# Performance work log

Measured on AMD Instinct MI355X. Metric: run time of the kernel, lower is better.

The kernel has to match this reference:

```python
import jax, jax.numpy as jnp
import numpy as np

B, S = 1, 1536
D_MODEL, NHEAD, HEAD_DIM = 1024, 16, 64
ROPE, NUM_SEQ = 32, 4
KVC, QC, D_FF = 256, 384, 4096
SPP = S // NUM_SEQ                      # seq per stock = 384
EPS_RMS = 1.1920929e-07                 # torch RMSNorm default eps = finfo(fp32).eps
ATTN_EPS = 1e-5
LAMBDA_INIT = 0.8 - 0.6 * float(np.exp(-0.3 * 0.0))  # depth 0 -> 0.2
SCALING = float(((HEAD_DIM + ROPE) // 2) ** -0.5)


def rmsnorm(x, w, eps=EPS_RMS):
    var = jnp.mean(jnp.square(x), axis=-1, keepdims=True)
    return x * jax.lax.rsqrt(var + eps) * w


def setup_inputs() -> dict:
    key = jax.random.key(0)
    ks = jax.random.split(key, 16)
    sd = 0.02
    inv_freq = 1.0 / (10000.0 ** (np.arange(0, ROPE // 4) / (ROPE // 4)))
    ang = np.arange(1, SPP)[:, None] * inv_freq[None, :]  # [SPP-1, ROPE//4]
    return {
        "x": jax.random.normal(ks[0], (B, S, D_MODEL), jnp.float32),
        "freqs_cos": jnp.asarray(np.cos(ang), jnp.float32),
        "freqs_sin": jnp.asarray(np.sin(ang), jnp.float32),
        "norm1_w": jnp.ones((D_MODEL,), jnp.float32),
        "norm2_w": jnp.ones((D_MODEL,), jnp.float32),
        "kv_down_w": jax.random.normal(ks[1], (KVC + ROPE, D_MODEL), jnp.float32) * sd,
        "q_down_w": jax.random.normal(ks[2], (QC, D_MODEL), jnp.float32) * sd,
        "kv_norm_w": jnp.ones((KVC,), jnp.float32),
        "q_norm_w": jnp.ones((QC,), jnp.float32),
        "kv_up_w": jax.random.normal(ks[3], (HEAD_DIM * NHEAD * 2, KVC), jnp.float32) * sd,
        "q_up_w": jax.random.normal(ks[4], ((HEAD_DIM + ROPE) * NHEAD, QC), jnp.float32) * sd,
        "lambda_q1": jax.random.normal(ks[5], (HEAD_DIM // 2,), jnp.float32) * 0.1,
        "lambda_k1": jax.random.normal(ks[6], (HEAD_DIM // 2,), jnp.float32) * 0.1,
        "lambda_q2": jax.random.normal(ks[7], (HEAD_DIM // 2,), jnp.float32) * 0.1,
        "lambda_k2": jax.random.normal(ks[8], (HEAD_DIM // 2,), jnp.float32) * 0.1,
        "attn_norm_w": jnp.ones((HEAD_DIM,), jnp.float32),
        "o_w": jax.random.normal(ks[9], (D_MODEL, NHEAD * HEAD_DIM), jnp.float32) * sd,
        "ff_in_w": jax.random.normal(ks[10], (D_FF * 2, D_MODEL), jnp.float32) * sd,
        "ff_out_w": jax.random.normal(ks[11], (D_MODEL, D_FF), jnp.float32) * sd,
    }


def reference(x, freqs_cos, freqs_sin, norm1_w, norm2_w, kv_down_w, q_down_w,
              kv_norm_w, q_norm_w, kv_up_w, q_up_w, lambda_q1, lambda_k1,
              lambda_q2, lambda_k2, attn_norm_w, o_w, ff_in_w, ff_out_w):
    b, s, _ = x.shape
    spp = s // NUM_SEQ
    H2, hd2 = 2 * NHEAD, HEAD_DIM // 2

    # block-tiled causal mask (1 = masked), matching mask.repeat(..., num_seq, num_seq)
    base = jnp.triu(jnp.ones((spp, spp), jnp.float32), 1)
    mask = jnp.tile(base, (NUM_SEQ, NUM_SEQ))  # [S, S]

    xin = rmsnorm(x, norm1_w)
    ckv = xin @ kv_down_w.T                                    # [B,S,KVC+ROPE]
    c_kv, k_rope = ckv[..., :KVC], ckv[..., KVC:]
    kv = (rmsnorm(c_kv, kv_norm_w) @ kv_up_w.T).reshape(b, s, NHEAD, 2 * HEAD_DIM)
    k, v = kv[..., :HEAD_DIM], kv[..., HEAD_DIM:]
    k = k.reshape(b, s, H2, hd2)
    qf = (rmsnorm(xin @ q_down_w.T, q_norm_w) @ q_up_w.T).reshape(b, s, NHEAD, HEAD_DIM + ROPE)
    q, q_rope = qf[..., :HEAD_DIM], qf[..., HEAD_DIM:]
    q = q.reshape(b, s, H2, hd2)
    k_rope = jnp.tile(k_rope[:, :, None, :], (1, 1, NHEAD, 1)).reshape(b, s, H2, ROPE // 2)
    q_rope = q_rope.reshape(b, s, H2, ROPE // 2)

    # rotary emb; position 0 of every ticker is left untouched (identity rotation)
    cos = jnp.concatenate([jnp.ones((1, ROPE // 4), freqs_cos.dtype), freqs_cos], 0)  # [spp, ROPE//4]
    sin = jnp.concatenate([jnp.zeros((1, ROPE // 4), freqs_sin.dtype), freqs_sin], 0)

    def rot(r):
        # S is laid out as (position, ticker) interleaved: s = p*NUM_SEQ + t
        r = r.reshape(b, spp, NUM_SEQ, H2, ROPE // 4, 2)
        c = cos[None, :, None, None, :]
        s_ = sin[None, :, None, None, :]
        r0, r1 = r[..., 0], r[..., 1]
        y = jnp.stack([r0 * c - r1 * s_, r0 * s_ + r1 * c], axis=-1)
        return y.reshape(b, s, H2, ROPE // 2)

    q = jnp.concatenate([q, rot(q_rope)], -1).transpose(0, 2, 1, 3)  # [B,2H,S,dk]
    k = jnp.concatenate([k, rot(k_rope)], -1).transpose(0, 2, 1, 3)
    v = v.transpose(0, 2, 1, 3)                                      # [B,H,S,hd]

    a = jnp.einsum('bhqd,bhkd->bhqk', q, k) * SCALING
    a = jnp.where(mask[None, None] == 1, -1e9, a)
    a = jax.nn.softmax(a, axis=-1)

    lam = jnp.exp(jnp.sum(lambda_k1 * lambda_q1)) - jnp.exp(jnp.sum(lambda_k2 * lambda_q2)) + LAMBDA_INIT
    a = a.reshape(b, NHEAD, 2, s, s)
    a1, a2 = a[:, :, 0], a[:, :, 1]
    g = jnp.mean(a1, axis=-2, keepdims=True)            # [B,H,1,S], broadcasts over queries
    a = a1 - lam * a2 + lam * g
    a = jnp.where(mask[None, None] == 1, 0.0, a)

    out = jnp.einsum('bhqk,bhkd->bhqd', a, v)           # [B,H,S,hd]
    out = rmsnorm(out.transpose(0, 2, 1, 3), attn_norm_w, eps=ATTN_EPS).transpose(0, 2, 1, 3)
    # faithful to source: raw reshape of [B,H,S,hd] -> [B,S,H*hd] (transposes cancel)
    out = out.reshape(b, s, NHEAD * HEAD_DIM)
    x = x + out @ o_w.T

    h = rmsnorm(x, norm2_w)
    uv = h @ ff_in_w.T
    u, vg = uv[..., :D_FF], uv[..., D_FF:]
    return x + (u * jax.nn.silu(vg)) @ ff_out_w.T
```

## Files before the change

### kernel.cpp

```cpp
#include <hip/hip_runtime.h>
#include <math.h>

#define S     1536
#define DM    1024
#define NH    16
#define H2N   32
#define HD    64
#define KVC   256
#define QC    384
#define DFF   4096
#define SPP   384
#define DQK   48
#define CKW   672
#define EPS_RMS  1.1920929e-07f
#define ATTN_EPS 1e-5f
#define SCALING  0.14433756729740643f

typedef float f32x4 __attribute__((ext_vector_type(4)));
typedef float f32x16 __attribute__((ext_vector_type(16)));
typedef short bf16x8 __attribute__((ext_vector_type(8)));

__device__ __forceinline__ short cvt_bf16(float f) {
  union { float f; unsigned u; } x; x.f = f;
  unsigned r = x.u + 0x7FFFu + ((x.u >> 16) & 1u);
  return (short)(r >> 16);
}
__device__ __forceinline__ unsigned pk2(float a, float b) {
  unsigned r;
  asm("v_cvt_pk_bf16_f32 %0, %1, %2" : "=v"(r) : "v"(a), "v"(b));
  return r;
}
__device__ __forceinline__ bf16x8 cvt8(float4 a, float4 b) {
  union { unsigned u[4]; bf16x8 v; } r;
  r.u[0] = pk2(a.x, a.y); r.u[1] = pk2(a.z, a.w);
  r.u[2] = pk2(b.x, b.y); r.u[3] = pk2(b.z, b.w);
  return r.v;
}
__device__ __forceinline__ int swz8(int flat, int nwg) {
  if (nwg & 7) return flat;
  return (flat & 7) * (nwg >> 3) + (flat >> 3);
}

__device__ __forceinline__ void rms_body(const float* xr, const float* w,
    short* yr, int cols, float eps) {
  const int tid = threadIdx.x;
  float ss = 0.f;
  for (int c = tid << 2; c < cols; c += 1024) {
    float4 v = *reinterpret_cast<const float4*>(xr + c);
    ss += v.x*v.x + v.y*v.y + v.z*v.z + v.w*v.w;
  }
#pragma unroll
  for (int mm = 1; mm < 64; mm <<= 1) ss += __shfl_xor(ss, mm, 64);
  __shared__ float red[4];
  if ((tid & 63) == 0) red[tid >> 6] = ss;
  __syncthreads();
  float tot = red[0] + red[1] + red[2] + red[3];
  float scale = rsqrtf(tot / (float)cols + eps);
  for (int c = tid << 2; c < cols; c += 1024) {
    float4 v = *reinterpret_cast<const float4*>(xr + c);
    float4 wv = *reinterpret_cast<const float4*>(w + c);
    uint2 p;
    p.x = pk2(v.x*scale*wv.x, v.y*scale*wv.y);
    p.y = pk2(v.z*scale*wv.z, v.w*scale*wv.w);
    *reinterpret_cast<uint2*>(yr + c) = p;
  }
}

__global__ __launch_bounds__(256) void rms1_cvt(const float* __restrict__ x,
    const float* __restrict__ n1w, short* __restrict__ xin_bf,
    const float* __restrict__ s0, int n0, const float* __restrict__ s1, int n1,
    const float* __restrict__ s2, int n2, const float* __restrict__ s3,
    short* __restrict__ dst) {
  const int bx = blockIdx.x;
  if (bx < S) {
    rms_body(x + (size_t)bx * DM, n1w, xin_bf + (size_t)bx * DM, DM, EPS_RMS);
  } else {
    long base = (long)(bx - S) * 2048 + (long)threadIdx.x * 8;
    const float* src; long off;
    if (base < n0) { src = s0; off = base; }
    else if (base < (long)n0 + n1) { src = s1; off = base - n0; }
    else if (base < (long)n0 + n1 + n2) { src = s2; off = base - n0 - n1; }
    else { src = s3; off = base - n0 - n1 - n2; }
    float4 a = *reinterpret_cast<const float4*>(src + off);
    float4 b = *reinterpret_cast<const float4*>(src + off + 4);
    *reinterpret_cast<bf16x8*>(dst + base) = cvt8(a, b);
  }
}

__global__ __launch_bounds__(256) void rmsnorm2_bf(const float* __restrict__ comb,
    const float* __restrict__ w0, const float* __restrict__ w1,
    short* __restrict__ o0, short* __restrict__ o1, float eps) {
  const int row = blockIdx.x;
  const int seg = blockIdx.y;
  const float* xr = comb + (size_t)row * CKW + (seg ? 288 : 0);
  rms_body(xr, seg ? w1 : w0,
           seg ? (o1 + (size_t)row * QC) : (o0 + (size_t)row * KVC),
           seg ? QC : KVC, eps);
}

__global__ __launch_bounds__(256) void rmsnorm_sum_bf(const float* __restrict__ p0,
    const float* __restrict__ p1, const float* __restrict__ xres,
    const float* __restrict__ w, float* __restrict__ outw, short* __restrict__ yb,
    float eps) {
  const int row = blockIdx.x;
  const int c = threadIdx.x << 2;
  const size_t base = (size_t)row * DM + c;
  float4 a = *reinterpret_cast<const float4*>(p0 + base);
  float4 b = *reinterpret_cast<const float4*>(p1 + base);
  float4 xv = *reinterpret_cast<const float4*>(xres + base);
  float4 v = make_float4(a.x+b.x+xv.x, a.y+b.y+xv.y, a.z+b.z+xv.z, a.w+b.w+xv.w);
  *reinterpret_cast<float4*>(outw + base) = v;
  float ss = v.x*v.x + v.y*v.y + v.z*v.z + v.w*v.w;
#pragma unroll
  for (int mm = 1; mm < 64; mm <<= 1) ss += __shfl_xor(ss, mm, 64);
  __shared__ float red[4];
  if ((threadIdx.x & 63) == 0) red[threadIdx.x >> 6] = ss;
  __syncthreads();
  float tot = red[0] + red[1] + red[2] + red[3];
  float scale = rsqrtf(tot * (1.0f / (float)DM) + eps);
  float4 wv = *reinterpret_cast<const float4*>(w + c);
  uint2 p;
  p.x = pk2(v.x*scale*wv.x, v.y*scale*wv.y);
  p.y = pk2(v.z*scale*wv.z, v.w*scale*wv.w);
  *reinterpret_cast<uint2*>(yb + base) = p;
}

__global__ __launch_bounds__(256) void fadd2(float* __restrict__ out,
    const float* __restrict__ p0, const float* __restrict__ p1) {
  size_t i = ((size_t)blockIdx.x * 256 + threadIdx.x) << 2;
  float4 o = *reinterpret_cast<float4*>(out + i);
  float4 a = *reinterpret_cast<const float4*>(p0 + i);
  float4 b = *reinterpret_cast<const float4*>(p1 + i);
  o.x += a.x + b.x; o.y += a.y + b.y; o.z += a.z + b.z; o.w += a.w + b.w;
  *reinterpret_cast<float4*>(out + i) = o;
}

template<int ADD>
__global__ __launch_bounds__(256) void mgemm_nt(const short* __restrict__ A,
    const short* __restrict__ B, const float* __restrict__ src, float* __restrict__ C,
    int M, int N, int K, int lda, int ldb, int ldc) {
  __shared__ short As[64][72];
  __shared__ short Bs[64][72];
  const int nwg = gridDim.x * gridDim.y;
  const int sfl = swz8(blockIdx.y * gridDim.x + blockIdx.x, nwg);
  const int bxs = sfl % gridDim.x, bys = sfl / gridDim.x;
  const int bm = bys * 64, bn = bxs * 64;
  const int tid = threadIdx.x;
  const int w = tid >> 6, lane = tid & 63;
  const int wr = (w >> 1) << 5, wc = (w & 1) << 5;
  const int srow = tid >> 2, sk = (tid & 3) << 4;
  const int lrow = lane & 15, lk8 = (lane >> 4) << 3;
  const int arow = bm + srow, brow = bn + srow;
  const bool bvalid = brow < N;
  f32x4 acc[2][2];
#pragma unroll
  for (int i = 0; i < 2; ++i)
#pragma unroll
    for (int j = 0; j < 2; ++j) acc[i][j] = (f32x4){0.f, 0.f, 0.f, 0.f};

  bf16x8 rah0, rah1, rbh0, rbh1;
  {
    const short* ap = A + (size_t)arow * lda + sk;
    rah0 = *reinterpret_cast<const bf16x8*>(ap);
    rah1 = *reinterpret_cast<const bf16x8*>(ap + 8);
  }
  rbh0 = (bf16x8){0,0,0,0,0,0,0,0}; rbh1 = rbh0;
  if (bvalid) {
    const short* bp = B + (size_t)brow * ldb + sk;
    rbh0 = *reinterpret_cast<const bf16x8*>(bp);
    rbh1 = *reinterpret_cast<const bf16x8*>(bp + 8);
  }

  for (int k0 = 0; k0 < K; k0 += 64) {
    bf16x8 va0 = rah0, va1 = rah1, vb0 = rbh0, vb1 = rbh1;
    __syncthreads();
    *reinterpret_cast<bf16x8*>(&As[srow][sk])     = va0;
    *reinterpret_cast<bf16x8*>(&As[srow][sk + 8]) = va1;
    *reinterpret_cast<bf16x8*>(&Bs[srow][sk])     = vb0;
    *reinterpret_cast<bf16x8*>(&Bs[srow][sk + 8]) = vb1;
    __syncthreads();
    const int kn = k0 + 64;
    if (kn < K) {
      const short* ap = A + (size_t)arow * lda + kn + sk;
      rah0 = *reinterpret_cast<const bf16x8*>(ap);
      rah1 = *reinterpret_cast<const bf16x8*>(ap + 8);
      if (bvalid) {
        const short* bp = B + (size_t)brow * ldb + kn + sk;
        rbh0 = *reinterpret_cast<const bf16x8*>(bp);
        rbh1 = *reinterpret_cast<const bf16x8*>(bp + 8);
      }
    }
#pragma unroll
    for (int kk = 0; kk < 2; ++kk) {
      bf16x8 af0 = *reinterpret_cast<bf16x8*>(&As[wr + lrow][(kk << 5) + lk8]);
      bf16x8 af1 = *reinterpret_cast<bf16x8*>(&As[wr + 16 + lrow][(kk << 5) + lk8]);
      bf16x8 bf0 = *reinterpret_cast<bf16x8*>(&Bs[wc + lrow][(kk << 5) + lk8]);
      bf16x8 bf1 = *reinterpret_cast<bf16x8*>(&Bs[wc + 16 + lrow][(kk << 5) + lk8]);
      acc[0][0] = __builtin_amdgcn_mfma_f32_16x16x32_bf16(af0, bf0, acc[0][0], 0, 0, 0);
      acc[0][1] = __builtin_amdgcn_mfma_f32_16x16x32_bf16(af0, bf1, acc[0][1], 0, 0, 0);
      acc[1][0] = __builtin_amdgcn_mfma_f32_16x16x32_bf16(af1, bf0, acc[1][0], 0, 0, 0);
      acc[1][1] = __builtin_amdgcn_mfma_f32_16x16x32_bf16(af1, bf1, acc[1][1], 0, 0, 0);
    }
  }
  const int crow0 = bm + wr + ((lane >> 4) << 2);
  const int ccol0 = bn + wc + lrow;
#pragma unroll
  for (int mi = 0; mi < 2; ++mi)
#pragma unroll
    for (int ni = 0; ni < 2; ++ni) {
      int colc = ccol0 + (ni << 4);
      if (colc < N) {
#pragma unroll
        for (int r = 0; r < 4; ++r) {
          int rowc = crow0 + (mi << 4) + r;
          float v = acc[mi][ni][r];
          if (ADD) v += src[(size_t)rowc * ldc + colc];
          C[(size_t)rowc * ldc + colc] = v;
        }
      }
    }
}

__global__ __launch_bounds__(256) void mgemm_dual(const short* __restrict__ A0,
    const short* __restrict__ B0, float* __restrict__ C0,
    const short* __restrict__ A1, const short* __restrict__ B1, float* __restrict__ C1) {
  __shared__ short As[64][72];
  __shared__ short Bs[64][72];
  const int flat = blockIdx.x;
  const short *A, *B; float* C;
  int K, lda, ldb, ldc, bm, bn;
  if (flat < 768) {
    const int sfl = swz8(flat, 768);
    bm = (sfl / 32) * 64; bn = (sfl % 32) * 64;
    A = A0; B = B0; C = C0; K = KVC; lda = KVC; ldb = KVC; ldc = 2048;
  } else {
    const int sfl = swz8(flat - 768, 576);
    bm = (sfl / 24) * 64; bn = (sfl % 24) * 64;
    A = A1; B = B1; C = C1; K = QC; lda = QC; ldb = QC; ldc = 1536;
  }
  const int tid = threadIdx.x;
  const int w = tid >> 6, lane = tid & 63;
  const int wr = (w >> 1) << 5, wc = (w & 1) << 5;
  const int srow = tid >> 2, sk = (tid & 3) << 4;
  const int lrow = lane & 15, lk8 = (lane >> 4) << 3;
  const int arow = bm + srow, brow = bn + srow;
  f32x4 acc[2][2];
#pragma unroll
  for (int i = 0; i < 2; ++i)
#pragma unroll
    for (int j = 0; j < 2; ++j) acc[i][j] = (f32x4){0.f, 0.f, 0.f, 0.f};

  bf16x8 rah0, rah1, rbh0, rbh1;
  {
    const short* ap = A + (size_t)arow * lda + sk;
    rah0 = *reinterpret_cast<const bf16x8*>(ap);
    rah1 = *reinterpret_cast<const bf16x8*>(ap + 8);
    const short* bp = B + (size_t)brow * ldb + sk;
    rbh0 = *reinterpret_cast<const bf16x8*>(bp);
    rbh1 = *reinterpret_cast<const bf16x8*>(bp + 8);
  }
  for (int k0 = 0; k0 < K; k0 += 64) {
    bf16x8 va0 = rah0, va1 = rah1, vb0 = rbh0, vb1 = rbh1;
    __syncthreads();
    *reinterpret_cast<bf16x8*>(&As[srow][sk])     = va0;
    *reinterpret_cast<bf16x8*>(&As[srow][sk + 8]) = va1;
    *reinterpret_cast<bf16x8*>(&Bs[srow][sk])     = vb0;
    *reinterpret_cast<bf16x8*>(&Bs[srow][sk + 8]) = vb1;
    __syncthreads();
    const int kn = k0 + 64;
    if (kn < K) {
      const short* ap = A + (size_t)arow * lda + kn + sk;
      rah0 = *reinterpret_cast<const bf16x8*>(ap);
      rah1 = *reinterpret_cast<const bf16x8*>(ap + 8);
      const short* bp = B + (size_t)brow * ldb + kn + sk;
      rbh0 = *reinterpret_cast<const bf16x8*>(bp);
      rbh1 = *reinterpret_cast<const bf16x8*>(bp + 8);
    }
#pragma unroll
    for (int kk = 0; kk < 2; ++kk) {
      bf16x8 af0 = *reinterpret_cast<bf16x8*>(&As[wr + lrow][(kk << 5) + lk8]);
      bf16x8 af1 = *reinterpret_cast<bf16x8*>(&As[wr + 16 + lrow][(kk << 5) + lk8]);
      bf16x8 bf0 = *reinterpret_cast<bf16x8*>(&Bs[wc + lrow][(kk << 5) + lk8]);
      bf16x8 bf1 = *reinterpret_cast<bf16x8*>(&Bs[wc + 16 + lrow][(kk << 5) + lk8]);
      acc[0][0] = __builtin_amdgcn_mfma_f32_16x16x32_bf16(af0, bf0, acc[0][0], 0, 0, 0);
      acc[0][1] = __builtin_amdgcn_mfma_f32_16x16x32_bf16(af0, bf1, acc[0][1], 0, 0, 0);
      acc[1][0] = __builtin_amdgcn_mfma_f32_16x16x32_bf16(af1, bf0, acc[1][0], 0, 0, 0);
      acc[1][1] = __builtin_amdgcn_mfma_f32_16x16x32_bf16(af1, bf1, acc[1][1], 0, 0, 0);
    }
  }
  const int crow0 = bm + wr + ((lane >> 4) << 2);
  const int ccol0 = bn + wc + lrow;
#pragma unroll
  for (int mi = 0; mi < 2; ++mi)
#pragma unroll
    for (int ni = 0; ni < 2; ++ni) {
      int colc = ccol0 + (ni << 4);
#pragma unroll
      for (int r = 0; r < 4; ++r) {
        int rowc = crow0 + (mi << 4) + r;
        C[(size_t)rowc * ldc + colc] = acc[mi][ni][r];
      }
    }
}

__device__ __forceinline__ void sk_body(const short* __restrict__ A,
    const short* __restrict__ B, float* __restrict__ C,
    int bm, int bn, int koff, int K2, int lda, int ldb, int ldc) {
  __shared__ short As[64][72];
  __shared__ short Bs[64][72];
  const int tid = threadIdx.x;
  const int w = tid >> 6, lane = tid & 63;
  const int wr = (w >> 1) << 5, wc = (w & 1) << 5;
  const int srow = tid >> 2, sk = (tid & 3) << 4;
  const int lrow = lane & 15, lk8 = (lane >> 4) << 3;
  const int arow = bm + srow, brow = bn + srow;
  f32x4 acc[2][2];
#pragma unroll
  for (int i = 0; i < 2; ++i)
#pragma unroll
    for (int j = 0; j < 2; ++j) acc[i][j] = (f32x4){0.f, 0.f, 0.f, 0.f};

  bf16x8 rah0, rah1, rbh0, rbh1;
  {
    const short* ap = A + (size_t)arow * lda + koff + sk;
    rah0 = *reinterpret_cast<const bf16x8*>(ap);
    rah1 = *reinterpret_cast<const bf16x8*>(ap + 8);
    const short* bp = B + (size_t)brow * ldb + koff + sk;
    rbh0 = *reinterpret_cast<const bf16x8*>(bp);
    rbh1 = *reinterpret_cast<const bf16x8*>(bp + 8);
  }
  const int kend = koff + K2;
  for (int k0 = koff; k0 < kend; k0 += 64) {
    bf16x8 va0 = rah0, va1 = rah1, vb0 = rbh0, vb1 = rbh1;
    __syncthreads();
    *reinterpret_cast<bf16x8*>(&As[srow][sk])     = va0;
    *reinterpret_cast<bf16x8*>(&As[srow][sk + 8]) = va1;
    *reinterpret_cast<bf16x8*>(&Bs[srow][sk])     = vb0;
    *reinterpret_cast<bf16x8*>(&Bs[srow][sk + 8]) = vb1;
    __syncthreads();
    const int kn = k0 + 64;
    if (kn < kend) {
      const short* ap = A + (size_t)arow * lda + kn + sk;
      rah0 = *reinterpret_cast<const bf16x8*>(ap);
      rah1 = *reinterpret_cast<const bf16x8*>(ap + 8);
      const short* bp = B + (size_t)brow * ldb + kn + sk;
      rbh0 = *reinterpret_cast<const bf16x8*>(bp);
      rbh1 = *reinterpret_cast<const bf16x8*>(bp + 8);
    }
#pragma unroll
    for (int kk = 0; kk < 2; ++kk) {
      bf16x8 af0 = *reinterpret_cast<bf16x8*>(&As[wr + lrow][(kk << 5) + lk8]);
      bf16x8 af1 = *reinterpret_cast<bf16x8*>(&As[wr + 16 + lrow][(kk << 5) + lk8]);
      bf16x8 bf0 = *reinterpret_cast<bf16x8*>(&Bs[wc + lrow][(kk << 5) + lk8]);
      bf16x8 bf1 = *reinterpret_cast<bf16x8*>(&Bs[wc + 16 + lrow][(kk << 5) + lk8]);
      acc[0][0] = __builtin_amdgcn_mfma_f32_16x16x32_bf16(af0, bf0, acc[0][0], 0, 0, 0);
      acc[0][1] = __builtin_amdgcn_mfma_f32_16x16x32_bf16(af0, bf1, acc[0][1], 0, 0, 0);
      acc[1][0] = __builtin_amdgcn_mfma_f32_16x16x32_bf16(af1, bf0, acc[1][0], 0, 0, 0);
      acc[1][1] = __builtin_amdgcn_mfma_f32_16x16x32_bf16(af1, bf1, acc[1][1], 0, 0, 0);
    }
  }
  const int crow0 = bm + wr + ((lane >> 4) << 2);
  const int ccol0 = bn + wc + lrow;
#pragma unroll
  for (int mi = 0; mi < 2; ++mi)
#pragma unroll
    for (int ni = 0; ni < 2; ++ni) {
      int colc = ccol0 + (ni << 4);
#pragma unroll
      for (int r = 0; r < 4; ++r) {
        int rowc = crow0 + (mi << 4) + r;
        C[(size_t)rowc * ldc + colc] = acc[mi][ni][r];
      }
    }
}

__global__ __launch_bounds__(256) void mgemm_sk(const short* __restrict__ A,
    const short* __restrict__ B, float* __restrict__ P0, float* __restrict__ P1,
    int M, int N, int K2, int lda, int ldb, int ldc) {
  const int nwg = gridDim.x * gridDim.y;
  const int sfl = swz8(blockIdx.y * gridDim.x + blockIdx.x, nwg);
  sk_body(A, B, blockIdx.z ? P1 : P0, (sfl / gridDim.x) * 64,
          (sfl % gridDim.x) * 64, blockIdx.z * K2, K2, lda, ldb, ldc);
}

__global__ __launch_bounds__(256) void oproj_cvt(const short* __restrict__ A,
    const short* __restrict__ B, float* __restrict__ P0, float* __restrict__ P1,
    const float* __restrict__ ffow, short* __restrict__ ffow_bf) {
  const int bx = blockIdx.x;
  if (bx < 768) {
    const int z = bx >= 384;
    const int sfl = swz8(bx - (z ? 384 : 0), 384);
    sk_body(A, B, z ? P1 : P0, (sfl / 16) * 64, (sfl % 16) * 64,
            z * 512, 512, DM, DM, DM);
  } else {
    long base = (long)(bx - 768) * 2048 + (long)threadIdx.x * 8;
    float4 a = *reinterpret_cast<const float4*>(ffow + base);
    float4 b = *reinterpret_cast<const float4*>(ffow + base + 4);
    *reinterpret_cast<bf16x8*>(ffow_bf + base) = cvt8(a, b);
  }
}

__global__ __launch_bounds__(256) void mgemm_glu(const short* __restrict__ A,
    const short* __restrict__ Bw, short* __restrict__ C,
    int M, int N, int K, int lda, int ldb, int ldc) {
  __shared__ short As[128][72];
  __shared__ short Bu[64][72];
  __shared__ short Bv[64][72];
  const int nwg = gridDim.x * gridDim.y;
  const int sfl = swz8(blockIdx.y * gridDim.x + blockIdx.x, nwg);
  const int bxs = sfl % gridDim.x, bys = sfl / gridDim.x;
  const int bm = bys * 128, bn = bxs * 64;
  const int tid = threadIdx.x;
  const int w = tid >> 6, lane = tid & 63;
  const int wr = (w >> 1) << 6, wc = (w & 1) << 5;
  const int arow = bm + (tid >> 1), ac = (tid & 1) << 5;
  const int brow = bn + (tid >> 2), bc = (tid & 3) << 4;
  const int lrow = lane & 15, lk8 = (lane >> 4) << 3;
  f32x4 au[4][2], av[4][2];
#pragma unroll
  for (int i = 0; i < 4; ++i)
#pragma unroll
    for (int j = 0; j < 2; ++j) {
      au[i][j] = (f32x4){0.f, 0.f, 0.f, 0.f};
      av[i][j] = (f32x4){0.f, 0.f, 0.f, 0.f};
    }
  bf16x8 ra[4], ru[2], rv[2];
  {
    const short* ap = A + (size_t)arow * lda + ac;
    const short* up = Bw + (size_t)brow * ldb + bc;
    const short* vp = Bw + (size_t)(N + brow) * ldb + bc;
#pragma unroll
    for (int e = 0; e < 4; ++e) ra[e] = *reinterpret_cast<const bf16x8*>(ap + (e << 3));
    ru[0] = *reinterpret_cast<const bf16x8*>(up);
    ru[1] = *reinterpret_cast<const bf16x8*>(up + 8);
    rv[0] = *reinterpret_cast<const bf16x8*>(vp);
    rv[1] = *reinterpret_cast<const bf16x8*>(vp + 8);
  }
  for (int k0 = 0; k0 < K; k0 += 64) {
    __syncthreads();
#pragma unroll
    for (int e = 0; e < 4; ++e)
      *reinterpret_cast<bf16x8*>(&As[tid >> 1][ac + (e << 3)]) = ra[e];
    *reinterpret_cast<bf16x8*>(&Bu[tid >> 2][bc])     = ru[0];
    *reinterpret_cast<bf16x8*>(&Bu[tid >> 2][bc + 8]) = ru[1];
    *reinterpret_cast<bf16x8*>(&Bv[tid >> 2][bc])     = rv[0];
    *reinterpret_cast<bf16x8*>(&Bv[tid >> 2][bc + 8]) = rv[1];
    __syncthreads();
    const int kn = k0 + 64;
    if (kn < K) {
      const short* ap = A + (size_t)arow * lda + kn + ac;
      const short* up = Bw + (size_t)brow * ldb + kn + bc;
      const short* vp = Bw + (size_t)(N + brow) * ldb + kn + bc;
#pragma unroll
      for (int e = 0; e < 4; ++e) ra[e] = *reinterpret_cast<const bf16x8*>(ap + (e << 3));
      ru[0] = *reinterpret_cast<const bf16x8*>(up);
      ru[1] = *reinterpret_cast<const bf16x8*>(up + 8);
      rv[0] = *reinterpret_cast<const bf16x8*>(vp);
      rv[1] = *reinterpret_cast<const bf16x8*>(vp + 8);
    }
#pragma unroll
    for (int kk = 0; kk < 2; ++kk) {
      bf16x8 af[4], uf[2], vf[2];
#pragma unroll
      for (int i = 0; i < 4; ++i)
        af[i] = *reinterpret_cast<bf16x8*>(&As[wr + (i << 4) + lrow][(kk << 5) + lk8]);
#pragma unroll
      for (int j = 0; j < 2; ++j) {
        uf[j] = *reinterpret_cast<bf16x8*>(&Bu[wc + (j << 4) + lrow][(kk << 5) + lk8]);
        vf[j] = *reinterpret_cast<bf16x8*>(&Bv[wc + (j << 4) + lrow][(kk << 5) + lk8]);
      }
      __builtin_amdgcn_s_setprio(1);
#pragma unroll
      for (int i = 0; i < 4; ++i)
#pragma unroll
        for (int j = 0; j < 2; ++j) {
          au[i][j] = __builtin_amdgcn_mfma_f32_16x16x32_bf16(af[i], uf[j], au[i][j], 0, 0, 0);
          av[i][j] = __builtin_amdgcn_mfma_f32_16x16x32_bf16(af[i], vf[j], av[i][j], 0, 0, 0);
        }
      __builtin_amdgcn_s_setprio(0);
    }
  }
  const int crow0 = bm + wr + ((lane >> 4) << 2);
  const int ccol0 = bn + wc + lrow;
#pragma unroll
  for (int mi = 0; mi < 4; ++mi)
#pragma unroll
    for (int ni = 0; ni < 2; ++ni) {
      int colc = ccol0 + (ni << 4);
#pragma unroll
      for (int r = 0; r < 4; ++r) {
        int rowc = crow0 + (mi << 4) + r;
        float uu = au[mi][ni][r], vg = av[mi][ni][r];
        float sig = 1.0f / (1.0f + __expf(-vg));
        C[(size_t)rowc * ldc + colc] = cvt_bf16(uu * vg * sig);
      }
    }
}

__global__ __launch_bounds__(256) void prep_attn(const float* __restrict__ qf,
    const float* __restrict__ kvb, const float* __restrict__ ckv,
    const float* __restrict__ fc, const float* __restrict__ fs,
    short* __restrict__ Qb, short* __restrict__ Kb, short* __restrict__ Vt) {
  __shared__ short Ts[128][74];
  const int bx = blockIdx.x;
  if (bx < 192) {
    const int t = (bx % 6) * 256 + threadIdx.x;
    const int h2 = bx / 6;
    const int hh = h2 >> 1, par = h2 & 1;
    const float* qrow = qf + (size_t)t*1536 + hh*96;
    const float* krow = kvb + (size_t)t*2048 + hh*128;
    unsigned qu[24], ku[24];
#pragma unroll
    for (int xq = 0; xq < 8; ++xq) {
      float4 qv = *reinterpret_cast<const float4*>(qrow + par*32 + (xq<<2));
      float4 kv = *reinterpret_cast<const float4*>(krow + par*32 + (xq<<2));
      qu[xq*2]   = pk2(qv.x, qv.y); qu[xq*2+1] = pk2(qv.z, qv.w);
      ku[xq*2]   = pk2(kv.x, kv.y); ku[xq*2+1] = pk2(kv.z, kv.w);
    }
    int p = t >> 2;
    const float* qr = qrow + 64 + par*16;
    const float* kr = ckv + (size_t)t*CKW + 256 + par*16;
#pragma unroll
    for (int mq = 0; mq < 8; ++mq) {
      float c = 1.f, sn = 0.f;
      if (p > 0) { c = fc[(p-1)*8 + mq]; sn = fs[(p-1)*8 + mq]; }
      float q0 = qr[2*mq], q1 = qr[2*mq+1];
      qu[16 + mq] = pk2(q0*c - q1*sn, q0*sn + q1*c);
      float k0 = kr[2*mq], k1 = kr[2*mq+1];
      ku[16 + mq] = pk2(k0*c - k1*sn, k0*sn + k1*c);
    }
    unsigned* qo = (unsigned*)(Qb + ((size_t)h2*S + t)*DQK);
    unsigned* ko = (unsigned*)(Kb + ((size_t)h2*S + t)*DQK);
#pragma unroll
    for (int e = 0; e < 6; ++e) {
      *reinterpret_cast<uint4*>(qo + (e<<2)) = make_uint4(qu[e*4], qu[e*4+1], qu[e*4+2], qu[e*4+3]);
      *reinterpret_cast<uint4*>(ko + (e<<2)) = make_uint4(ku[e*4], ku[e*4+1], ku[e*4+2], ku[e*4+3]);
    }
  } else {
    const int f2 = bx - 192;
    const int hh = f2 % 16;
    const int t0 = (f2 / 16) << 7;
    const int tl = threadIdx.x >> 3, dp = (threadIdx.x & 7) << 3;
#pragma unroll
    for (int pass = 0; pass < 4; ++pass) {
      int t = t0 + (pass << 5) + tl;
      const float* vp = kvb + (size_t)t*2048 + hh*128 + 64 + dp;
      float4 a = *reinterpret_cast<const float4*>(vp);
      float4 b = *reinterpret_cast<const float4*>(vp + 4);
      *reinterpret_cast<bf16x8*>(&Ts[(pass << 5) + tl][dp]) = cvt8(a, b);
    }
    __syncthreads();
    for (int idx = threadIdx.x; idx < 1024; idx += 256) {
      int d = idx >> 4, tseg = (idx & 15) << 3;
      bf16x8 v;
#pragma unroll
      for (int e = 0; e < 8; ++e) v[e] = Ts[tseg + e][d];
      *reinterpret_cast<bf16x8*>(Vt + ((size_t)hh*HD + d)*S + t0 + tseg) = v;
    }
  }
}

__global__ __launch_bounds__(256) void flash_mfma(const short* __restrict__ Qb,
    const short* __restrict__ Kb, const short* __restrict__ Vg,
    float* __restrict__ Ob, float* __restrict__ rowm, float* __restrict__ rowl,
    float* __restrict__ Ob1a, float* __restrict__ Ob1b,
    float* __restrict__ rm1, float* __restrict__ rl1) {
  const int h2 = blockIdx.y;
  const int hh = h2 >> 1;
  const int z  = blockIdx.z;
  const int tid = threadIdx.x;
  const int w = tid >> 6, lane = tid & 63;
  const int ql = lane & 31, h = lane >> 5;
  const int cq = blockIdx.x / 3, k = blockIdx.x % 3;
  const int qi = k + 3*w;
  const int qbase = cq*SPP + (qi << 5);
  const int ri0w = qi << 5;

  __shared__ __align__(16) float Ot[4][32][36];

  bf16x8 qf0, qf1, qf2;
  {
    const short* qp = Qb + ((size_t)h2*S + qbase + ql)*DQK + (h << 3);
    qf0 = *reinterpret_cast<const bf16x8*>(qp);
    qf1 = *reinterpret_cast<const bf16x8*>(qp + 16);
    qf2 = *reinterpret_cast<const bf16x8*>(qp + 32);
  }
  const short* Kbase = Kb + (size_t)h2*S*DQK + (h << 3);
  const short* V0 = Vg + ((size_t)hh*HD + ql)*S + (h << 3);
  const short* V1 = Vg + ((size_t)hh*HD + 32 + ql)*S + (h << 3);

  float m = -1e30f, l = 0.f;
  f32x16 o0, o1;
#pragma unroll
  for (int r = 0; r < 16; ++r) { o0[r] = 0.f; o1[r] = 0.f; }

  for (int c = (z << 1); c < (z << 1) + 2; ++c) {
    for (int jr = 0; jr <= ri0w; jr += 32) {
      const int j0 = c*SPP + jr;
      const bool diag = (jr == ri0w);
      const short* kp = Kbase + (size_t)(j0 + ql)*DQK;
      bf16x8 kf0 = *reinterpret_cast<const bf16x8*>(kp);
      bf16x8 kf1 = *reinterpret_cast<const bf16x8*>(kp + 16);
      bf16x8 kf2 = *reinterpret_cast<const bf16x8*>(kp + 32);
      bf16x8 v00 = *reinterpret_cast<const bf16x8*>(V0 + j0);
      bf16x8 v01 = *reinterpret_cast<const bf16x8*>(V0 + j0 + 16);
      bf16x8 v10 = *reinterpret_cast<const bf16x8*>(V1 + j0);
      bf16x8 v11 = *reinterpret_cast<const bf16x8*>(V1 + j0 + 16);

      f32x16 st;
#pragma unroll
      for (int r = 0; r < 16; ++r) st[r] = 0.f;
      __builtin_amdgcn_s_setprio(1);
      st = __builtin_amdgcn_mfma_f32_32x32x16_bf16(kf0, qf0, st, 0, 0, 0);
      st = __builtin_amdgcn_mfma_f32_32x32x16_bf16(kf1, qf1, st, 0, 0, 0);
      st = __builtin_amdgcn_mfma_f32_32x32x16_bf16(kf2, qf2, st, 0, 0, 0);
      __builtin_amdgcn_s_setprio(0);

      if (diag) {
#pragma unroll
        for (int r = 0; r < 16; ++r) {
          int kl = (r & 3) + ((r >> 2) << 3) + (h << 2);
          st[r] = (kl <= ql) ? st[r] * SCALING : -1e30f;
        }
      } else {
#pragma unroll
        for (int r = 0; r < 16; ++r) st[r] *= SCALING;
      }

      float tm = st[0];
#pragma unroll
      for (int r = 1; r < 16; ++r) tm = fmaxf(tm, st[r]);
      tm = fmaxf(tm, __shfl_xor(tm, 32));
      if (__any(tm > m + 8.0f)) {
        float mnew = fmaxf(m, tm);
        float sc = __expf(m - mnew);
        m = mnew;
        l *= sc;
#pragma unroll
        for (int r = 0; r < 16; ++r) { o0[r] *= sc; o1[r] *= sc; }
      }
      float ps = 0.f;
#pragma unroll
      for (int r = 0; r < 16; ++r) { float p = __expf(st[r] - m); st[r] = p; ps += p; }
      ps += __shfl_xor(ps, 32);
      l += ps;

      unsigned A0 = pk2(st[0],  st[1]),  B0 = pk2(st[2],  st[3]);
      unsigned C0 = pk2(st[4],  st[5]),  D0 = pk2(st[6],  st[7]);
      unsigned A1 = pk2(st[8],  st[9]),  B1 = pk2(st[10], st[11]);
      unsigned C1 = pk2(st[12], st[13]), D1 = pk2(st[14], st[15]);
      unsigned xA0 = (unsigned)__shfl_xor((int)A0, 32), xB0 = (unsigned)__shfl_xor((int)B0, 32);
      unsigned xC0 = (unsigned)__shfl_xor((int)C0, 32), xD0 = (unsigned)__shfl_xor((int)D0, 32);
      unsigned xA1 = (unsigned)__shfl_xor((int)A1, 32), xB1 = (unsigned)__shfl_xor((int)B1, 32);
      unsigned xC1 = (unsigned)__shfl_xor((int)C1, 32), xD1 = (unsigned)__shfl_xor((int)D1, 32);
      union { unsigned u[4]; bf16x8 v; } P0, P1;
      P0.u[0] = h ? xC0 : A0;  P0.u[1] = h ? xD0 : B0;
      P0.u[2] = h ? C0 : xA0;  P0.u[3] = h ? D0 : xB0;
      P1.u[0] = h ? xC1 : A1;  P1.u[1] = h ? xD1 : B1;
      P1.u[2] = h ? C1 : xA1;  P1.u[3] = h ? D1 : xB1;

      __builtin_amdgcn_s_setprio(1);
      o0 = __builtin_amdgcn_mfma_f32_32x32x16_bf16(v00, P0.v, o0, 0, 0, 0);
      o0 = __builtin_amdgcn_mfma_f32_32x32x16_bf16(v01, P1.v, o0, 0, 0, 0);
      o1 = __builtin_amdgcn_mfma_f32_32x32x16_bf16(v10, P0.v, o1, 0, 0, 0);
      o1 = __builtin_amdgcn_mfma_f32_32x32x16_bf16(v11, P1.v, o1, 0, 0, 0);
      __builtin_amdgcn_s_setprio(0);
    }
  }

  float* ot = &Ot[w][0][0];
  float* orow;
  if (z == 0) orow = Ob + ((size_t)h2*S + qbase)*HD;
  else orow = (h2 < 16) ? Ob1a + ((size_t)h2*S + qbase)*HD
                        : Ob1b + ((size_t)(h2 - 16)*S + qbase)*HD;
#pragma unroll
  for (int r = 0; r < 16; ++r) {
    int dl = (r & 3) + ((r >> 2) << 3) + (h << 2);
    ot[ql*36 + dl] = o0[r];
  }
#pragma unroll
  for (int it = 0; it < 4; ++it) {
    int idx = lane + (it << 6);
    int row = idx >> 3, c4 = (idx & 7) << 2;
    float4 v = *reinterpret_cast<float4*>(&ot[row*36 + c4]);
    *reinterpret_cast<float4*>(&orow[(size_t)row*HD + c4]) = v;
  }
#pragma unroll
  for (int r = 0; r < 16; ++r) {
    int dl = (r & 3) + ((r >> 2) << 3) + (h << 2);
    ot[ql*36 + dl] = o1[r];
  }
#pragma unroll
  for (int it = 0; it < 4; ++it) {
    int idx = lane + (it << 6);
    int row = idx >> 3, c4 = (idx & 7) << 2;
    float4 v = *reinterpret_cast<float4*>(&ot[row*36 + c4]);
    *reinterpret_cast<float4*>(&orow[(size_t)row*HD + 32 + c4]) = v;
  }
  if (lane < 32) {
    if (z == 0) { rowm[h2*S + qbase + lane] = m; rowl[h2*S + qbase + lane] = l; }
    else        { rm1[h2*S + qbase + lane] = m;  rl1[h2*S + qbase + lane] = l; }
  }
}

__global__ __launch_bounds__(256) void merge_ml(float* __restrict__ rowm,
    float* __restrict__ rowl, float* __restrict__ rm1, float* __restrict__ rl1,
    const float* __restrict__ lq1, const float* __restrict__ lk1,
    const float* __restrict__ lq2, const float* __restrict__ lk2,
    float* __restrict__ lamp) {
  const int gid = blockIdx.x * 256 + threadIdx.x;
  float m0 = rowm[gid], l0 = rowl[gid], m1 = rm1[gid], l1 = rl1[gid];
  float m = fmaxf(m0, m1);
  float w0 = __expf(m0 - m), w1 = __expf(m1 - m);
  float L = l0*w0 + l1*w1;
  float linv = 1.0f / L;
  rowm[gid] = m; rowl[gid] = L;
  rm1[gid] = w0 * linv; rl1[gid] = w1 * linv;
  if (blockIdx.x == 0 && threadIdx.x < 32) {
    int t = threadIdx.x;
    float a = lq1[t]*lk1[t];
    float b = lq2[t]*lk2[t];
#pragma unroll
    for (int mm = 1; mm < 32; mm <<= 1) { a += __shfl_xor(a, mm, 32); b += __shfl_xor(b, mm, 32); }
    if (t == 0) lamp[0] = expf(a) - expf(b) + 0.2f;
  }
}

__global__ __launch_bounds__(256) void colsum_mfma(const short* __restrict__ Qb,
    const short* __restrict__ Kb, const float* __restrict__ rowm,
    const float* __restrict__ rowl, float* __restrict__ gcol) {
  const int jt = blockIdx.x;
  const int hh = blockIdx.y, h2 = hh << 1;
  const int cK = jt / 12, jr32 = jt % 12;
  const int jr = jr32 << 5;
  const int j0 = cK*SPP + jr;
  const int tid = threadIdx.x;
  const int w = tid >> 6, lane = tid & 63;
  const int ql = lane & 31, h = lane >> 5;

  bf16x8 kf0, kf1, kf2;
  {
    const short* kp = Kb + ((size_t)h2*S + j0 + ql)*DQK + (h << 3);
    kf0 = *reinterpret_cast<const bf16x8*>(kp);
    kf1 = *reinterpret_cast<const bf16x8*>(kp + 16);
    kf2 = *reinterpret_cast<const bf16x8*>(kp + 32);
  }
  const int nt = 12 - jr32;
  const int T = nt << 2;
  float gs[16];
#pragma unroll
  for (int r = 0; r < 16; ++r) gs[r] = 0.f;

  for (int tt = w; tt < T; tt += 4) {
    int cq = tt / nt, qrem = tt - cq*nt;
    int qi = jr32 + qrem;
    int i0 = cq*SPP + (qi << 5);
    const bool diag = (qrem == 0);
    const short* qp = Qb + ((size_t)h2*S + i0 + ql)*DQK + (h << 3);
    bf16x8 qf0 = *reinterpret_cast<const bf16x8*>(qp);
    bf16x8 qf1 = *reinterpret_cast<const bf16x8*>(qp + 16);
    bf16x8 qf2 = *reinterpret_cast<const bf16x8*>(qp + 32);
    f32x16 st;
#pragma unroll
    for (int r = 0; r < 16; ++r) st[r] = 0.f;
    __builtin_amdgcn_s_setprio(1);
    st = __builtin_amdgcn_mfma_f32_32x32x16_bf16(kf0, qf0, st, 0, 0, 0);
    st = __builtin_amdgcn_mfma_f32_32x32x16_bf16(kf1, qf1, st, 0, 0, 0);
    st = __builtin_amdgcn_mfma_f32_32x32x16_bf16(kf2, qf2, st, 0, 0, 0);
    __builtin_amdgcn_s_setprio(0);
    float Mq = rowm[h2*S + i0 + ql];
    float Lq = 1.0f / rowl[h2*S + i0 + ql];
    if (diag) {
#pragma unroll
      for (int r = 0; r < 16; ++r) {
        int kl = (r & 3) + ((r >> 2) << 3) + (h << 2);
        if (kl <= ql) gs[r] += __expf(st[r]*SCALING - Mq) * Lq;
      }
    } else {
#pragma unroll
      for (int r = 0; r < 16; ++r) gs[r] += __expf(st[r]*SCALING - Mq) * Lq;
    }
  }
  __shared__ float gw[4][32];
#pragma unroll
  for (int r = 0; r < 16; ++r) {
    float v = gs[r];
#pragma unroll
    for (int mm = 1; mm < 32; mm <<= 1) v += __shfl_xor(v, mm, 32);
    if (ql == 0) gw[w][(r & 3) + ((r >> 2) << 3) + (h << 2)] = v;
  }
  __syncthreads();
  if (tid < 32) {
    float s = gw[0][tid] + gw[1][tid] + gw[2][tid] + gw[3][tid];
    gcol[hh*S + j0 + tid] = s * (1.0f / (float)S);
  }
}

__global__ __launch_bounds__(256) void wpre_cvt(const float* __restrict__ gcol,
    const float* __restrict__ kvb, float* __restrict__ Wpre,
    const float* __restrict__ ffiw, const float* __restrict__ ow,
    short* __restrict__ ffiw_bf) {
  const int bx = blockIdx.x;
  if (bx >= 64) {
    long base = (long)(bx - 64) * 2048 + (long)threadIdx.x * 8;
    const float* src; long off;
    if (base < 8388608L) { src = ffiw; off = base; }
    else { src = ow; off = base - 8388608L; }
    float4 a = *reinterpret_cast<const float4*>(src + off);
    float4 b = *reinterpret_cast<const float4*>(src + off + 4);
    *reinterpret_cast<bf16x8*>(ffiw_bf + base) = cvt8(a, b);
    return;
  }
  const int hh = bx >> 2;
  const int dq = (bx & 3) << 4;
  __shared__ float Wt[SPP][16];
  const int tid = threadIdx.x;
  for (int idx = tid; idx < SPP*16; idx += 256) {
    int r = idx >> 4, dd = idx & 15;
    float val = 0.f;
#pragma unroll
    for (int b2 = 0; b2 < 4; ++b2) {
      int j = b2*SPP + r;
      val = fmaf(gcol[hh*S + j], kvb[(size_t)j*2048 + hh*128 + 64 + dq + dd], val);
    }
    Wt[r][dd] = val;
  }
  __syncthreads();
  if (tid < 16) {
    float run = 0.f;
    for (int r = 0; r < SPP; ++r) { run += Wt[r][tid]; Wt[r][tid] = run; }
  }
  __syncthreads();
  for (int idx = tid; idx < SPP*16; idx += 256) {
    int r = idx >> 4, dd = idx & 15;
    Wpre[((size_t)hh*SPP + r)*HD + dq + dd] = Wt[r][dd];
  }
}

__global__ __launch_bounds__(256) void combine_rms(const float* __restrict__ Ob,
    const float* __restrict__ Ob1a, const float* __restrict__ Ob1b,
    const float* __restrict__ a0v, const float* __restrict__ a1v,
    const float* __restrict__ Wpre, const float* __restrict__ lamp,
    const float* __restrict__ anw, short* __restrict__ attno) {
  const int t = blockIdx.x * 4 + (threadIdx.x >> 6);
  const int h = blockIdx.y;
  const int d = threadIdx.x & 63;
  const float lam = lamp[0];
  const int g1 = (2*h)*S + t, g2 = (2*h+1)*S + t;
  const float* p1 = (h < 8) ? (Ob1a + (size_t)g1*HD) : (Ob1b + ((size_t)g1 - (size_t)16*S)*HD);
  const float* p2 = (h < 8) ? (Ob1a + (size_t)g2*HD) : (Ob1b + ((size_t)g2 - (size_t)16*S)*HD);
  float o1 = Ob[(size_t)g1*HD + d] * a0v[g1] + p1[d] * a1v[g1];
  float o2 = Ob[(size_t)g2*HD + d] * a0v[g2] + p2[d] * a1v[g2];
  const float w3 = Wpre[((size_t)h*SPP + (t % SPP))*HD + d];
  float val = o1 - lam*o2 + lam*w3;
  float ss = val*val;
#pragma unroll
  for (int mm = 1; mm < 64; mm <<= 1) ss += __shfl_xor(ss, mm, 64);
  float scale = rsqrtf(ss * (1.0f/HD) + ATTN_EPS) * anw[d];
  int tn = h*96 + (t >> 4);
  int cn = ((t & 15) << 6) + d;
  attno[(size_t)tn*DM + cn] = cvt_bf16(val * scale);
}

extern "C" void kernel_launch(void* const* d_in, const int* in_sizes, int n_in,
                              void* d_out, int out_size, void* d_ws, size_t ws_size,
                              hipStream_t stream) {
  (void)in_sizes; (void)n_in; (void)out_size;
  const float* x    = (const float*)d_in[0];
  const float* fc   = (const float*)d_in[1];
  const float* fs   = (const float*)d_in[2];
  const float* n1w  = (const float*)d_in[3];
  const float* n2w  = (const float*)d_in[4];
  const float* kvdw = (const float*)d_in[5];
  const float* qdw  = (const float*)d_in[6];
  const float* kvnw = (const float*)d_in[7];
  const float* qnw  = (const float*)d_in[8];
  const float* kvuw = (const float*)d_in[9];
  const float* quw  = (const float*)d_in[10];
  const float* lq1  = (const float*)d_in[11];
  const float* lk1  = (const float*)d_in[12];
  const float* lq2  = (const float*)d_in[13];
  const float* lk2  = (const float*)d_in[14];
  const float* anw  = (const float*)d_in[15];
  const float* ow   = (const float*)d_in[16];
  const float* ffiw = (const float*)d_in[17];
  const float* ffow = (const float*)d_in[18];
  float* out = (float*)d_out;
  float* ws  = (float*)d_ws;

  float* xin   = ws;
  float* ckv   = xin   + (size_t)S*DM;
  float* qmid  = ckv   + (size_t)S*288;
  float* kvb   = qmid  + (size_t)S*QC;
  float* qf    = kvb   + (size_t)S*2048;
  float* Qb    = qf    + (size_t)S*1536;
  float* Kb    = Qb    + (size_t)H2N*S*DQK;
  float* Obuf  = Kb    + (size_t)H2N*S*DQK;
  float* rowm  = Obuf  + (size_t)H2N*S*HD;
  float* rowl  = rowm  + (size_t)H2N*S;
  float* gcol  = rowl  + (size_t)H2N*S;
  float* Wpre  = gcol  + (size_t)NH*S;
  float* attno = Wpre  + (size_t)NH*SPP*HD;
  float* lamp  = attno + (size_t)S*DM;
  short* fbufs = (short*)kvb;
  float* Ob1a = xin;
  float* Ob1b = qf;
  float* rm1  = qf + (size_t)16*S*HD;
  float* rl1  = rm1 + (size_t)H2N*S;
  short* Qb_bf = (short*)Qb;
  short* Kb_bf = (short*)Kb;
  short* Vt_bf = (short*)Qb + 2359296;
  short* xin_bf  = (short*)xin;
  short* ckv_bf  = (short*)Obuf;
  short* qmid_bf = ckv_bf + (size_t)S*KVC;
  short* h_bf    = (short*)ckv;
  short* attno_bf = (short*)attno;
  short* kvdw_bf = (short*)attno;
  short* qdw_bf  = kvdw_bf + 294912;
  short* kvuw_bf = qdw_bf  + 393216;
  short* quw_bf  = kvuw_bf + 524288;
  short* ffiw_bf = (short*)Qb;
  short* ow_bf   = ffiw_bf + 8388608;
  short* ffow_bf = (short*)Obuf;
  float* psum0 = xin;
  float* psum1 = qf;
  if (ws_size < (size_t)18063376 * sizeof(float)) return;

  rms1_cvt<<<S + 880, 256, 0, stream>>>(x, n1w, xin_bf,
      kvdw, 294912, qdw, 393216, kvuw, 524288, quw, kvdw_bf);
  { dim3 g(11, 24); mgemm_nt<0><<<g, 256, 0, stream>>>(xin_bf, kvdw_bf, nullptr, ckv, S, CKW, DM, DM, DM, CKW); }
  { dim3 g(S, 2);   rmsnorm2_bf<<<g, 256, 0, stream>>>(ckv, kvnw, qnw, ckv_bf, qmid_bf, EPS_RMS); }
  mgemm_dual<<<1344, 256, 0, stream>>>(ckv_bf, kvuw_bf, kvb, qmid_bf, quw_bf, qf);
  prep_attn<<<384, 256, 0, stream>>>(qf, kvb, ckv, fc, fs, Qb_bf, Kb_bf, Vt_bf);
  { dim3 g(12, 32, 2); flash_mfma<<<g, 256, 0, stream>>>(Qb_bf, Kb_bf, Vt_bf, Obuf, rowm, rowl,
                                                         Ob1a, Ob1b, rm1, rl1); }
  merge_ml<<<(H2N*S)/256, 256, 0, stream>>>(rowm, rowl, rm1, rl1, lq1, lk1, lq2, lk2, lamp);
  { dim3 g(48, 16); colsum_mfma<<<g, 256, 0, stream>>>(Qb_bf, Kb_bf, rowm, rowl, gcol); }
  wpre_cvt<<<64 + 4608, 256, 0, stream>>>(gcol, kvb, Wpre, ffiw, ow, ffiw_bf);
  { dim3 g(S/4, 16); combine_rms<<<g, 256, 0, stream>>>(Obuf, Ob1a, Ob1b, rm1, rl1,
                                                        Wpre, lamp, anw, attno_bf); }
  oproj_cvt<<<768 + 2048, 256, 0, stream>>>(attno_bf, ow_bf, psum0, psum1, ffow, ffow_bf);
  rmsnorm_sum_bf<<<S, 256, 0, stream>>>(psum0, psum1, x, n2w, out, h_bf, EPS_RMS);
  { dim3 g(64, 12); mgemm_glu<<<g, 256, 0, stream>>>(h_bf, ffiw_bf, fbufs, S, DFF, DM, DM, DM, DFF); }
  { dim3 g(16, 24, 2); mgemm_sk<<<g, 256, 0, stream>>>(fbufs, ffow_bf, psum0, psum1, S, DM, 2048, DFF, DFF, DM); }
  fadd2<<<1536, 256, 0, stream>>>(out, psum0, psum1);
}
```

Measured before the change: 202.6 us.

## Remove merge_ml kernel by recomputing split-softmax merge in consumers and prescaling Q

The standalone merge_ml launch is dropped. Its lambda computation moves into an extra block of prep_attn, and the two-split max/sum merge is recomputed inline in colsum_mfma and combine_rms from the raw per-split statistics. The softmax scaling is also folded into Q when it is converted to bf16, which removes the per-element multiply in flash_mfma and colsum. This saves one kernel launch and a pass over the row statistics, at the cost of redundant exp/div work in the consumers and slightly different rounding from scaling before bf16 conversion.

```diff
diff --git a/kernel.cpp b/kernel.cpp
--- a/kernel.cpp
+++ b/kernel.cpp
@@ -500,7 +500,10 @@
 __global__ __launch_bounds__(256) void prep_attn(const float* __restrict__ qf,
     const float* __restrict__ kvb, const float* __restrict__ ckv,
     const float* __restrict__ fc, const float* __restrict__ fs,
-    short* __restrict__ Qb, short* __restrict__ Kb, short* __restrict__ Vt) {
+    short* __restrict__ Qb, short* __restrict__ Kb, short* __restrict__ Vt,
+    const float* __restrict__ lq1, const float* __restrict__ lk1,
+    const float* __restrict__ lq2, const float* __restrict__ lk2,
+    float* __restrict__ lamp) {
   __shared__ short Ts[128][74];
   const int bx = blockIdx.x;
   if (bx < 192) {
@@ -514,7 +517,8 @@
     for (int xq = 0; xq < 8; ++xq) {
       float4 qv = *reinterpret_cast<const float4*>(qrow + par*32 + (xq<<2));
       float4 kv = *reinterpret_cast<const float4*>(krow + par*32 + (xq<<2));
-      qu[xq*2]   = pk2(qv.x, qv.y); qu[xq*2+1] = pk2(qv.z, qv.w);
+      qu[xq*2]   = pk2(qv.x*SCALING, qv.y*SCALING);
+      qu[xq*2+1] = pk2(qv.z*SCALING, qv.w*SCALING);
       ku[xq*2]   = pk2(kv.x, kv.y); ku[xq*2+1] = pk2(kv.z, kv.w);
     }
     int p = t >> 2;
@@ -525,7 +529,7 @@
       float c = 1.f, sn = 0.f;
       if (p > 0) { c = fc[(p-1)*8 + mq]; sn = fs[(p-1)*8 + mq]; }
       float q0 = qr[2*mq], q1 = qr[2*mq+1];
-      qu[16 + mq] = pk2(q0*c - q1*sn, q0*sn + q1*c);
+      qu[16 + mq] = pk2((q0*c - q1*sn)*SCALING, (q0*sn + q1*c)*SCALING);
       float k0 = kr[2*mq], k1 = kr[2*mq+1];
       ku[16 + mq] = pk2(k0*c - k1*sn, k0*sn + k1*c);
     }
@@ -536,7 +540,7 @@
       *reinterpret_cast<uint4*>(qo + (e<<2)) = make_uint4(qu[e*4], qu[e*4+1], qu[e*4+2], qu[e*4+3]);
       *reinterpret_cast<uint4*>(ko + (e<<2)) = make_uint4(ku[e*4], ku[e*4+1], ku[e*4+2], ku[e*4+3]);
     }
-  } else {
+  } else if (bx < 384) {
     const int f2 = bx - 192;
     const int hh = f2 % 16;
     const int t0 = (f2 / 16) << 7;
@@ -557,6 +561,13 @@
       for (int e = 0; e < 8; ++e) v[e] = Ts[tseg + e][d];
       *reinterpret_cast<bf16x8*>(Vt + ((size_t)hh*HD + d)*S + t0 + tseg) = v;
     }
+  } else if (threadIdx.x < 32) {
+    int t = threadIdx.x;
+    float a = lq1[t]*lk1[t];
+    float b = lq2[t]*lk2[t];
+#pragma unroll
+    for (int mm = 1; mm < 32; mm <<= 1) { a += __shfl_xor(a, mm, 32); b += __shfl_xor(b, mm, 32); }
+    if (t == 0) lamp[0] = expf(a) - expf(b) + 0.2f;
   }
 }
 
@@ -620,11 +631,8 @@
 #pragma unroll
         for (int r = 0; r < 16; ++r) {
           int kl = (r & 3) + ((r >> 2) << 3) + (h << 2);
-          st[r] = (kl <= ql) ? st[r] * SCALING : -1e30f;
+          if (kl > ql) st[r] = -1e30f;
         }
-      } else {
-#pragma unroll
-        for (int r = 0; r < 16; ++r) st[r] *= SCALING;
       }
 
       float tm = st[0];
@@ -703,32 +711,10 @@
   }
 }
 
-__global__ __launch_bounds__(256) void merge_ml(float* __restrict__ rowm,
-    float* __restrict__ rowl, float* __restrict__ rm1, float* __restrict__ rl1,
-    const float* __restrict__ lq1, const float* __restrict__ lk1,
-    const float* __restrict__ lq2, const float* __restrict__ lk2,
-    float* __restrict__ lamp) {
-  const int gid = blockIdx.x * 256 + threadIdx.x;
-  float m0 = rowm[gid], l0 = rowl[gid], m1 = rm1[gid], l1 = rl1[gid];
-  float m = fmaxf(m0, m1);
-  float w0 = __expf(m0 - m), w1 = __expf(m1 - m);
-  float L = l0*w0 + l1*w1;
-  float linv = 1.0f / L;
-  rowm[gid] = m; rowl[gid] = L;
-  rm1[gid] = w0 * linv; rl1[gid] = w1 * linv;
-  if (blockIdx.x == 0 && threadIdx.x < 32) {
-    int t = threadIdx.x;
-    float a = lq1[t]*lk1[t];
-    float b = lq2[t]*lk2[t];
-#pragma unroll
-    for (int mm = 1; mm < 32; mm <<= 1) { a += __shfl_xor(a, mm, 32); b += __shfl_xor(b, mm, 32); }
-    if (t == 0) lamp[0] = expf(a) - expf(b) + 0.2f;
-  }
-}
-
 __global__ __launch_bounds__(256) void colsum_mfma(const short* __restrict__ Qb,
     const short* __restrict__ Kb, const float* __restrict__ rowm,
-    const float* __restrict__ rowl, float* __restrict__ gcol) {
+    const float* __restrict__ rowl, const float* __restrict__ rm1,
+    const float* __restrict__ rl1, float* __restrict__ gcol) {
   const int jt = blockIdx.x;
   const int hh = blockIdx.y, h2 = hh << 1;
   const int cK = jt / 12, jr32 = jt % 12;
@@ -768,17 +754,20 @@
     st = __builtin_amdgcn_mfma_f32_32x32x16_bf16(kf1, qf1, st, 0, 0, 0);
     st = __builtin_amdgcn_mfma_f32_32x32x16_bf16(kf2, qf2, st, 0, 0, 0);
     __builtin_amdgcn_s_setprio(0);
-    float Mq = rowm[h2*S + i0 + ql];
-    float Lq = 1.0f / rowl[h2*S + i0 + ql];
+    const int gidx = h2*S + i0 + ql;
+    float m0 = rowm[gidx], l0 = rowl[gidx], m1 = rm1[gidx], l1 = rl1[gidx];
+    float Mq = fmaxf(m0, m1);
+    float Lm = l0*__expf(m0 - Mq) + l1*__expf(m1 - Mq);
+    float Lq = 1.0f / Lm;
     if (diag) {
 #pragma unroll
       for (int r = 0; r < 16; ++r) {
         int kl = (r & 3) + ((r >> 2) << 3) + (h << 2);
-        if (kl <= ql) gs[r] += __expf(st[r]*SCALING - Mq) * Lq;
+        if (kl <= ql) gs[r] += __expf(st[r] - Mq) * Lq;
       }
     } else {
 #pragma unroll
-      for (int r = 0; r < 16; ++r) gs[r] += __expf(st[r]*SCALING - Mq) * Lq;
+      for (int r = 0; r < 16; ++r) gs[r] += __expf(st[r] - Mq) * Lq;
     }
   }
   __shared__ float gw[4][32];
@@ -839,7 +828,8 @@
 
 __global__ __launch_bounds__(256) void combine_rms(const float* __restrict__ Ob,
     const float* __restrict__ Ob1a, const float* __restrict__ Ob1b,
-    const float* __restrict__ a0v, const float* __restrict__ a1v,
+    const float* __restrict__ rowm, const float* __restrict__ rowl,
+    const float* __restrict__ rm1, const float* __restrict__ rl1,
     const float* __restrict__ Wpre, const float* __restrict__ lamp,
     const float* __restrict__ anw, short* __restrict__ attno) {
   const int t = blockIdx.x * 4 + (threadIdx.x >> 6);
@@ -849,8 +839,16 @@
   const int g1 = (2*h)*S + t, g2 = (2*h+1)*S + t;
   const float* p1 = (h < 8) ? (Ob1a + (size_t)g1*HD) : (Ob1b + ((size_t)g1 - (size_t)16*S)*HD);
   const float* p2 = (h < 8) ? (Ob1a + (size_t)g2*HD) : (Ob1b + ((size_t)g2 - (size_t)16*S)*HD);
-  float o1 = Ob[(size_t)g1*HD + d] * a0v[g1] + p1[d] * a1v[g1];
-  float o2 = Ob[(size_t)g2*HD + d] * a0v[g2] + p2[d] * a1v[g2];
+  float m10 = rowm[g1], l10 = rowl[g1], m11 = rm1[g1], l11 = rl1[g1];
+  float M1 = fmaxf(m10, m11);
+  float w10 = __expf(m10 - M1), w11 = __expf(m11 - M1);
+  float li1 = 1.0f / (l10*w10 + l11*w11);
+  float m20 = rowm[g2], l20 = rowl[g2], m21 = rm1[g2], l21 = rl1[g2];
+  float M2 = fmaxf(m20, m21);
+  float w20 = __expf(m20 - M2), w21 = __expf(m21 - M2);
+  float li2 = 1.0f / (l20*w20 + l21*w21);
+  float o1 = (Ob[(size_t)g1*HD + d] * w10 + p1[d] * w11) * li1;
+  float o2 = (Ob[(size_t)g2*HD + d] * w20 + p2[d] * w21) * li2;
   const float w3 = Wpre[((size_t)h*SPP + (t % SPP))*HD + d];
   float val = o1 - lam*o2 + lam*w3;
   float ss = val*val;
@@ -931,13 +929,13 @@
   { dim3 g(11, 24); mgemm_nt<0><<<g, 256, 0, stream>>>(xin_bf, kvdw_bf, nullptr, ckv, S, CKW, DM, DM, DM, CKW); }
   { dim3 g(S, 2);   rmsnorm2_bf<<<g, 256, 0, stream>>>(ckv, kvnw, qnw, ckv_bf, qmid_bf, EPS_RMS); }
   mgemm_dual<<<1344, 256, 0, stream>>>(ckv_bf, kvuw_bf, kvb, qmid_bf, quw_bf, qf);
-  prep_attn<<<384, 256, 0, stream>>>(qf, kvb, ckv, fc, fs, Qb_bf, Kb_bf, Vt_bf);
+  prep_attn<<<385, 256, 0, stream>>>(qf, kvb, ckv, fc, fs, Qb_bf, Kb_bf, Vt_bf,
+                                     lq1, lk1, lq2, lk2, lamp);
   { dim3 g(12, 32, 2); flash_mfma<<<g, 256, 0, stream>>>(Qb_bf, Kb_bf, Vt_bf, Obuf, rowm, rowl,
                                                          Ob1a, Ob1b, rm1, rl1); }
-  merge_ml<<<(H2N*S)/256, 256, 0, stream>>>(rowm, rowl, rm1, rl1, lq1, lk1, lq2, lk2, lamp);
-  { dim3 g(48, 16); colsum_mfma<<<g, 256, 0, stream>>>(Qb_bf, Kb_bf, rowm, rowl, gcol); }
+  { dim3 g(48, 16); colsum_mfma<<<g, 256, 0, stream>>>(Qb_bf, Kb_bf, rowm, rowl, rm1, rl1, gcol); }
   wpre_cvt<<<64 + 4608, 256, 0, stream>>>(gcol, kvb, Wpre, ffiw, ow, ffiw_bf);
-  { dim3 g(S/4, 16); combine_rms<<<g, 256, 0, stream>>>(Obuf, Ob1a, Ob1b, rm1, rl1,
+  { dim3 g(S/4, 16); combine_rms<<<g, 256, 0, stream>>>(Obuf, Ob1a, Ob1b, rowm, rowl, rm1, rl1,
                                                         Wpre, lamp, anw, attno_bf); }
   oproj_cvt<<<768 + 2048, 256, 0, stream>>>(attno_bf, ow_bf, psum0, psum1, ffow, ffow_bf);
   rmsnorm_sum_bf<<<S, 256, 0, stream>>>(psum0, psum1, x, n2w, out, h_bf, EPS_RMS);
```

Result: no change. 200.9 us (-0.9%).
